# Optimization experiments

Measured on AMD Instinct MI355X. Metric: run time of the kernel, lower is better.

The kernel has to match this reference:

```python
import jax, jax.numpy as jnp
import numpy as np

N = 50000      # nodes
E = 800000     # edges (avg degree 16)
IN_DIM, HID, OUT = 128, 128, 64
EPS = 1e-5     # BatchNorm1d eps


def setup_inputs() -> dict:
    key = jax.random.key(0)
    ks = jax.random.split(key, 8)
    x = jax.random.normal(ks[0], (N, IN_DIM), jnp.float32)
    edge_index = jax.random.randint(ks[1], (2, E), 0, N, dtype=jnp.int32)
    def lin(k, i, o):
        return jax.random.normal(k, (i, o), jnp.float32) / np.sqrt(i).astype(np.float32)
    return {
        "x": x,
        "edge_index": edge_index,
        "W1": lin(ks[2], IN_DIM, HID), "b1": jnp.zeros((HID,), jnp.float32),
        "g1": jnp.ones((HID,), jnp.float32), "beta1": jnp.zeros((HID,), jnp.float32),
        "W2": lin(ks[3], HID, HID), "b2": jnp.zeros((HID,), jnp.float32),
        "g2": jnp.ones((HID,), jnp.float32), "beta2": jnp.zeros((HID,), jnp.float32),
        "W3": lin(ks[4], HID, OUT), "b3": jnp.zeros((OUT,), jnp.float32),
    }


def reference(x, edge_index, W1, b1, g1, beta1, W2, b2, g2, beta2, W3, b3):
    # GCNConv normalization: add self-loops, sym norm D^-1/2 (A+I) D^-1/2
    loops = jnp.arange(N, dtype=edge_index.dtype)
    src = jnp.concatenate([edge_index[0], loops])  # message sources
    dst = jnp.concatenate([edge_index[1], loops])  # aggregation targets
    deg = jax.ops.segment_sum(jnp.ones_like(dst, jnp.float32), dst, num_segments=N)
    dis = jnp.where(deg > 0, jax.lax.rsqrt(jnp.maximum(deg, 1.0)), 0.0)
    norm = dis[src] * dis[dst]  # [E+N]

    def conv(h, W, b):
        h = h @ W  # lin before propagation (PyG GCNConv)
        agg = jax.ops.segment_sum(h[src] * norm[:, None], dst, num_segments=N)
        return agg + b  # bias after aggregation

    def bn(h, g, beta):
        # training-mode BatchNorm1d: batch stats over node dim (biased var)
        m = h.mean(axis=0)
        v = h.var(axis=0)
        return g * (h - m) * jax.lax.rsqrt(v + EPS) + beta

    h = jax.nn.relu(bn(conv(x, W1, b1), g1, beta1))   # dropout deterministic (identity)
    h = jax.nn.relu(bn(conv(h, W2, b2), g2, beta2))
    h = conv(h, W3, b3)
    return jax.nn.log_softmax(h, axis=-1)
```

## Files before the change

kernel.cpp:

```cpp
#include <hip/hip_runtime.h>
#include <hip/hip_fp16.h>
#include <math.h>

#define N_NODES 50000
#define N_EDGES 800000
#define BN_EPS 1e-5f
#define CAP 64

typedef _Float16 f16x8 __attribute__((ext_vector_type(8)));
typedef float f32x4 __attribute__((ext_vector_type(4)));

constexpr int GB = (N_NODES + 63) / 64;
constexpr int FB = 1536;
constexpr int AB = (N_NODES + 3) / 4;

__global__ void setup_k(const float* __restrict__ W1, const float* __restrict__ W2,
                        const float* __restrict__ W3, __half* __restrict__ Wt1,
                        __half* __restrict__ Wt2, __half* __restrict__ Wt3,
                        int* __restrict__ fil, float* __restrict__ sums) {
    int i = blockIdx.x * blockDim.x + threadIdx.x;
    if (i < N_NODES) fil[i] = 0;
    if (i < 512) sums[i] = 0.f;
    if (i < 16384) {
        int k = i >> 7, m = i & 127;
        Wt1[m * 128 + k] = __float2half(W1[i]);
        Wt2[m * 128 + k] = __float2half(W2[i]);
    }
    if (i < 8192) {
        int k = i >> 6, m = i & 63;
        Wt3[m * 128 + k] = __float2half(W3[i]);
    }
}

template <int M, int AF32, int FUSE>
__device__ __forceinline__ void gemm_body(int bid, int tid, __half* Ws,
                                          const void* __restrict__ Av,
                                          const __half* __restrict__ Wt,
                                          const float* __restrict__ scale,
                                          const float* __restrict__ shift,
                                          __half* __restrict__ out) {
    constexpr int NF = M / 32;
    int wid = tid >> 6, lane = tid & 63;

    for (int idx = tid; idx < M * 16; idx += 256) {
        int m = idx >> 4, c = idx & 15;
        *(float4*)(&Ws[m * 136 + c * 8]) = *(const float4*)(&Wt[m * 128 + c * 8]);
    }
    __syncthreads();

    int rbase = bid * 64 + (wid >> 1) * 32;
    int ncol0 = (wid & 1) * (M / 2);
    int koff = (lane >> 4) * 8;

    int arow[2];
#pragma unroll
    for (int mi = 0; mi < 2; ++mi) {
        int r = rbase + mi * 16 + (lane & 15);
        arow[mi] = (r < N_NODES) ? r : (N_NODES - 1);
    }

    f32x4 acc[2][NF];
#pragma unroll
    for (int mi = 0; mi < 2; ++mi)
#pragma unroll
        for (int ni = 0; ni < NF; ++ni) acc[mi][ni] = (f32x4)(0.f);

#pragma unroll
    for (int k0 = 0; k0 < 128; k0 += 32) {
        float scv[8], shv[8];
        if constexpr (FUSE) {
            *(float4*)scv = *(const float4*)(scale + k0 + koff);
            *(float4*)(scv + 4) = *(const float4*)(scale + k0 + koff + 4);
            *(float4*)shv = *(const float4*)(shift + k0 + koff);
            *(float4*)(shv + 4) = *(const float4*)(shift + k0 + koff + 4);
        }
        f16x8 a[2], b[NF];
#pragma unroll
        for (int mi = 0; mi < 2; ++mi) {
            if constexpr (AF32) {
                const float* Af = (const float*)Av + (size_t)arow[mi] * 128 + k0 + koff;
                float4 p0 = *(const float4*)Af;
                float4 p1 = *(const float4*)(Af + 4);
                a[mi][0] = (_Float16)p0.x; a[mi][1] = (_Float16)p0.y;
                a[mi][2] = (_Float16)p0.z; a[mi][3] = (_Float16)p0.w;
                a[mi][4] = (_Float16)p1.x; a[mi][5] = (_Float16)p1.y;
                a[mi][6] = (_Float16)p1.z; a[mi][7] = (_Float16)p1.w;
            } else {
                f16x8 raw = *(const f16x8*)((const __half*)Av + (size_t)arow[mi] * 128 + k0 + koff);
                if constexpr (FUSE) {
#pragma unroll
                    for (int j = 0; j < 8; ++j)
                        a[mi][j] = (_Float16)fmaxf((float)raw[j] * scv[j] + shv[j], 0.f);
                } else {
                    a[mi] = raw;
                }
            }
        }
#pragma unroll
        for (int ni = 0; ni < NF; ++ni)
            b[ni] = *(const f16x8*)(&Ws[(ncol0 + ni * 16 + (lane & 15)) * 136 + k0 + koff]);
#pragma unroll
        for (int mi = 0; mi < 2; ++mi)
#pragma unroll
            for (int ni = 0; ni < NF; ++ni)
                acc[mi][ni] = __builtin_amdgcn_mfma_f32_16x16x32_f16(a[mi], b[ni], acc[mi][ni], 0, 0, 0);
    }

    int ccol = ncol0 + (lane & 15);
#pragma unroll
    for (int mi = 0; mi < 2; ++mi)
#pragma unroll
        for (int q = 0; q < 4; ++q) {
            int grow = rbase + mi * 16 + (lane >> 4) * 4 + q;
            if (grow < N_NODES) {
#pragma unroll
                for (int ni = 0; ni < NF; ++ni)
                    out[(size_t)grow * M + ccol + ni * 16] = __float2half(acc[mi][ni][q]);
            }
        }
}

template <int M, int AF32, int FUSE>
__global__ __launch_bounds__(256) void mfma_gemm_k(const void* __restrict__ Av,
                                                   const __half* __restrict__ Wt,
                                                   const float* __restrict__ scale,
                                                   const float* __restrict__ shift,
                                                   __half* __restrict__ out) {
    __shared__ __half Ws[M * 136];
    gemm_body<M, AF32, FUSE>(blockIdx.x, threadIdx.x, Ws, Av, Wt, scale, shift, out);
}

__global__ __launch_bounds__(256) void gemm1_fill_k(const float* __restrict__ x,
                                                    const __half* __restrict__ Wt1,
                                                    __half* __restrict__ outh,
                                                    const int* __restrict__ ei,
                                                    int* __restrict__ fil,
                                                    int* __restrict__ bkt) {
    __shared__ __half Ws[128 * 136];
    if (blockIdx.x < GB) {
        gemm_body<128, 1, 0>(blockIdx.x, threadIdx.x, Ws, x, Wt1, nullptr, nullptr, outh);
    } else {
        int t = (blockIdx.x - GB) * 256 + threadIdx.x;
        for (int e = t; e < N_EDGES; e += FB * 256) {
            int src = ei[e], dst = ei[N_EDGES + e];
            int pos = atomicAdd(&fil[dst], 1);
            if (pos < CAP) bkt[dst * CAP + pos] = src;
        }
    }
}

__global__ __launch_bounds__(256) void aggh_k(const __half* __restrict__ hs,
                                              const int* __restrict__ fil,
                                              const int* __restrict__ bkt,
                                              const float* __restrict__ bias,
                                              __half* __restrict__ out) {
    int dst = blockIdx.x * 4 + (threadIdx.x >> 6);
    if (dst >= N_NODES) return;
    int lane = threadIdx.x & 63;
    int cnt = fil[dst];
    int n = min(cnt, CAP);
    float dd = rsqrtf((float)cnt + 1.f);
    const __half2* h2 = (const __half2*)hs;
    float2 v = __half22float2(h2[(size_t)dst * 64 + lane]);
    float ax = dd * v.x, ay = dd * v.y;
    const int* bp = bkt + (size_t)dst * CAP;
    int e = 0;
    for (; e + 4 <= n; e += 4) {
        int s0 = bp[e], s1 = bp[e + 1], s2 = bp[e + 2], s3 = bp[e + 3];
        float w0 = rsqrtf((float)fil[s0] + 1.f);
        float w1 = rsqrtf((float)fil[s1] + 1.f);
        float w2 = rsqrtf((float)fil[s2] + 1.f);
        float w3 = rsqrtf((float)fil[s3] + 1.f);
        float2 v0 = __half22float2(h2[(size_t)s0 * 64 + lane]);
        float2 v1 = __half22float2(h2[(size_t)s1 * 64 + lane]);
        float2 v2 = __half22float2(h2[(size_t)s2 * 64 + lane]);
        float2 v3 = __half22float2(h2[(size_t)s3 * 64 + lane]);
        ax += w0 * v0.x + w1 * v1.x + w2 * v2.x + w3 * v3.x;
        ay += w0 * v0.y + w1 * v1.y + w2 * v2.y + w3 * v3.y;
    }
    for (; e < n; ++e) {
        int s = bp[e];
        float w = rsqrtf((float)fil[s] + 1.f);
        float2 vv = __half22float2(h2[(size_t)s * 64 + lane]);
        ax += w * vv.x;
        ay += w * vv.y;
    }
    float2 b = *(const float2*)(bias + lane * 2);
    ((__half2*)out)[(size_t)dst * 64 + lane] =
        __float22half2_rn(make_float2(dd * ax + b.x, dd * ay + b.y));
}

__global__ __launch_bounds__(256) void stats_k(const __half* __restrict__ h,
                                               float* __restrict__ sum, float* __restrict__ sq) {
    __shared__ float ssum[128], ssq[128];
    int tid = threadIdx.x;
    if (tid < 128) { ssum[tid] = 0.f; ssq[tid] = 0.f; }
    __syncthreads();
    float s[8], q[8];
#pragma unroll
    for (int j = 0; j < 8; ++j) { s[j] = 0.f; q[j] = 0.f; }
    const int total = N_NODES * 16;
    int stride = gridDim.x * blockDim.x;
    for (int i = blockIdx.x * blockDim.x + tid; i < total; i += stride) {
        f16x8 v = ((const f16x8*)h)[i];
#pragma unroll
        for (int j = 0; j < 8; ++j) {
            float f = (float)v[j];
            s[j] += f;
            q[j] += f * f;
        }
    }
#pragma unroll
    for (int j = 0; j < 8; ++j) {
        s[j] += __shfl_xor(s[j], 16); s[j] += __shfl_xor(s[j], 32);
        q[j] += __shfl_xor(q[j], 16); q[j] += __shfl_xor(q[j], 32);
    }
    int lane = tid & 63;
    if (lane < 16) {
        int c0 = lane * 8;
#pragma unroll
        for (int j = 0; j < 8; ++j) {
            atomicAdd(&ssum[c0 + j], s[j]);
            atomicAdd(&ssq[c0 + j], q[j]);
        }
    }
    __syncthreads();
    if (tid < 128) {
        atomicAdd(&sum[tid], ssum[tid]);
        atomicAdd(&sq[tid], ssq[tid]);
    }
}

__global__ void finalize_k(const float* __restrict__ sum, const float* __restrict__ sq,
                           const float* __restrict__ g, const float* __restrict__ beta,
                           float* scale, float* shift) {
    int f = threadIdx.x;
    float m = sum[f] * (1.0f / N_NODES);
    float v = sq[f] * (1.0f / N_NODES) - m * m;
    float sc = g[f] * rsqrtf(v + BN_EPS);
    scale[f] = sc;
    shift[f] = beta[f] - m * sc;
}

__global__ __launch_bounds__(256) void agg64sm_k(const __half* __restrict__ hs,
                                                 const int* __restrict__ fil,
                                                 const int* __restrict__ bkt,
                                                 const float* __restrict__ bias,
                                                 float* __restrict__ out) {
    int dst = blockIdx.x * 4 + (threadIdx.x >> 6);
    if (dst >= N_NODES) return;
    int lane = threadIdx.x & 63;
    int cnt = fil[dst];
    int n = min(cnt, CAP);
    float dd = rsqrtf((float)cnt + 1.f);
    float acc = dd * __half2float(hs[(size_t)dst * 64 + lane]);
    const int* bp = bkt + (size_t)dst * CAP;
    int e = 0;
    for (; e + 4 <= n; e += 4) {
        int s0 = bp[e], s1 = bp[e + 1], s2 = bp[e + 2], s3 = bp[e + 3];
        float w0 = rsqrtf((float)fil[s0] + 1.f);
        float w1 = rsqrtf((float)fil[s1] + 1.f);
        float w2 = rsqrtf((float)fil[s2] + 1.f);
        float w3 = rsqrtf((float)fil[s3] + 1.f);
        float v0 = __half2float(hs[(size_t)s0 * 64 + lane]);
        float v1 = __half2float(hs[(size_t)s1 * 64 + lane]);
        float v2 = __half2float(hs[(size_t)s2 * 64 + lane]);
        float v3 = __half2float(hs[(size_t)s3 * 64 + lane]);
        acc += w0 * v0 + w1 * v1 + w2 * v2 + w3 * v3;
    }
    for (; e < n; ++e) {
        int s = bp[e];
        acc += rsqrtf((float)fil[s] + 1.f) * __half2float(hs[(size_t)s * 64 + lane]);
    }
    float v = dd * acc + bias[lane];
    float m = v;
#pragma unroll
    for (int off = 32; off; off >>= 1) m = fmaxf(m, __shfl_xor(m, off));
    float p = expf(v - m);
    float ssum = p;
#pragma unroll
    for (int off = 32; off; off >>= 1) ssum += __shfl_xor(ssum, off);
    out[(size_t)dst * 64 + lane] = v - m - logf(ssum);
}

extern "C" void kernel_launch(void* const* d_in, const int* in_sizes, int n_in,
                              void* d_out, int out_size, void* d_ws, size_t ws_size,
                              hipStream_t stream) {
    const float* x = (const float*)d_in[0];
    const int* ei = (const int*)d_in[1];
    const float* W1 = (const float*)d_in[2];
    const float* b1 = (const float*)d_in[3];
    const float* g1 = (const float*)d_in[4];
    const float* be1 = (const float*)d_in[5];
    const float* W2 = (const float*)d_in[6];
    const float* b2 = (const float*)d_in[7];
    const float* g2 = (const float*)d_in[8];
    const float* be2 = (const float*)d_in[9];
    const float* W3 = (const float*)d_in[10];
    const float* b3 = (const float*)d_in[11];
    float* out = (float*)d_out;

    char* p = (char*)d_ws;
    auto alloc = [&](size_t bytes) {
        void* r = (void*)p;
        p += (bytes + 255) & ~(size_t)255;
        return r;
    };
    int* fil = (int*)alloc(N_NODES * 4);
    int* bkt = (int*)alloc((size_t)N_NODES * CAP * 4);
    float* sums = (float*)alloc(512 * 4);
    float* ss = (float*)alloc(512 * 4);
    __half* Wt1 = (__half*)alloc(128 * 128 * 2);
    __half* Wt2 = (__half*)alloc(128 * 128 * 2);
    __half* Wt3 = (__half*)alloc(64 * 128 * 2);
    __half* bufP = (__half*)alloc((size_t)N_NODES * 128 * 2);
    __half* bufQ = (__half*)alloc((size_t)N_NODES * 128 * 2);

    setup_k<<<196, 256, 0, stream>>>(W1, W2, W3, Wt1, Wt2, Wt3, fil, sums);

    gemm1_fill_k<<<GB + FB, 256, 0, stream>>>(x, Wt1, bufQ, ei, fil, bkt);
    aggh_k<<<AB, 256, 0, stream>>>(bufQ, fil, bkt, b1, bufP);
    stats_k<<<1024, 256, 0, stream>>>(bufP, sums, sums + 128);
    finalize_k<<<1, 128, 0, stream>>>(sums, sums + 128, g1, be1, ss, ss + 128);

    mfma_gemm_k<128, 0, 1><<<GB, 256, 0, stream>>>(bufP, Wt2, ss, ss + 128, bufQ);
    aggh_k<<<AB, 256, 0, stream>>>(bufQ, fil, bkt, b2, bufP);
    stats_k<<<1024, 256, 0, stream>>>(bufP, sums + 256, sums + 384);
    finalize_k<<<1, 128, 0, stream>>>(sums + 256, sums + 384, g2, be2, ss + 256, ss + 384);

    mfma_gemm_k<64, 0, 1><<<GB, 256, 0, stream>>>(bufP, Wt3, ss + 256, ss + 384, bufQ);
    agg64sm_k<<<AB, 256, 0, stream>>>(bufQ, fil, bkt, b3, out);
}
```

Before: 281.5 us.

## Precompute degree norms, fold source scaling into GEMM epilogue, shrink bucket indices

Adds a kernel that precomputes D^-1/2 per node once. Layers 2 and 3 scale the GEMM output rows by the source normalisation, so the aggregation kernels no longer need per-edge weight gathers and reduce to plain sums. Bucket indices are stored as 16-bit values, which halves index traffic; this only holds because N fits in 16 bits. The GEMM now reads weights directly from global memory instead of staging them in LDS, and the fill/GEMM1 block order is swapped. Reading weights from global memory may cost extra load latency.

New measurement: 276.5 us. Within noise of the previous version (-1.8%).

```diff
diff --git a/kernel.cpp b/kernel.cpp
--- a/kernel.cpp
+++ b/kernel.cpp
@@ -32,21 +32,16 @@
     }
 }
 
-template <int M, int AF32, int FUSE>
-__device__ __forceinline__ void gemm_body(int bid, int tid, __half* Ws,
+template <int M, int AF32, int FUSE, int DSCALE>
+__device__ __forceinline__ void gemm_body(int bid, int tid,
                                           const void* __restrict__ Av,
                                           const __half* __restrict__ Wt,
                                           const float* __restrict__ scale,
                                           const float* __restrict__ shift,
+                                          const float* __restrict__ dis,
                                           __half* __restrict__ out) {
     constexpr int NF = M / 32;
     int wid = tid >> 6, lane = tid & 63;
-
-    for (int idx = tid; idx < M * 16; idx += 256) {
-        int m = idx >> 4, c = idx & 15;
-        *(float4*)(&Ws[m * 136 + c * 8]) = *(const float4*)(&Wt[m * 128 + c * 8]);
-    }
-    __syncthreads();
 
     int rbase = bid * 64 + (wid >> 1) * 32;
     int ncol0 = (wid & 1) * (M / 2);
@@ -98,7 +93,7 @@
         }
 #pragma unroll
         for (int ni = 0; ni < NF; ++ni)
-            b[ni] = *(const f16x8*)(&Ws[(ncol0 + ni * 16 + (lane & 15)) * 136 + k0 + koff]);
+            b[ni] = *(const f16x8*)(Wt + (size_t)(ncol0 + ni * 16 + (lane & 15)) * 128 + k0 + koff);
 #pragma unroll
         for (int mi = 0; mi < 2; ++mi)
 #pragma unroll
@@ -113,75 +108,86 @@
         for (int q = 0; q < 4; ++q) {
             int grow = rbase + mi * 16 + (lane >> 4) * 4 + q;
             if (grow < N_NODES) {
+                float ds = DSCALE ? dis[grow] : 1.0f;
 #pragma unroll
                 for (int ni = 0; ni < NF; ++ni)
-                    out[(size_t)grow * M + ccol + ni * 16] = __float2half(acc[mi][ni][q]);
+                    out[(size_t)grow * M + ccol + ni * 16] = __float2half(acc[mi][ni][q] * ds);
             }
         }
 }
 
-template <int M, int AF32, int FUSE>
+template <int M, int AF32, int FUSE, int DSCALE>
 __global__ __launch_bounds__(256) void mfma_gemm_k(const void* __restrict__ Av,
                                                    const __half* __restrict__ Wt,
                                                    const float* __restrict__ scale,
                                                    const float* __restrict__ shift,
+                                                   const float* __restrict__ dis,
                                                    __half* __restrict__ out) {
-    __shared__ __half Ws[M * 136];
-    gemm_body<M, AF32, FUSE>(blockIdx.x, threadIdx.x, Ws, Av, Wt, scale, shift, out);
-}
-
-__global__ __launch_bounds__(256) void gemm1_fill_k(const float* __restrict__ x,
+    gemm_body<M, AF32, FUSE, DSCALE>(blockIdx.x, threadIdx.x, Av, Wt, scale, shift, dis, out);
+}
+
+__global__ __launch_bounds__(256) void fill_gemm1_k(const float* __restrict__ x,
                                                     const __half* __restrict__ Wt1,
                                                     __half* __restrict__ outh,
                                                     const int* __restrict__ ei,
                                                     int* __restrict__ fil,
-                                                    int* __restrict__ bkt) {
-    __shared__ __half Ws[128 * 136];
-    if (blockIdx.x < GB) {
-        gemm_body<128, 1, 0>(blockIdx.x, threadIdx.x, Ws, x, Wt1, nullptr, nullptr, outh);
-    } else {
-        int t = (blockIdx.x - GB) * 256 + threadIdx.x;
+                                                    unsigned short* __restrict__ bkt) {
+    if (blockIdx.x < FB) {
+        int t = blockIdx.x * 256 + threadIdx.x;
         for (int e = t; e < N_EDGES; e += FB * 256) {
             int src = ei[e], dst = ei[N_EDGES + e];
             int pos = atomicAdd(&fil[dst], 1);
-            if (pos < CAP) bkt[dst * CAP + pos] = src;
-        }
-    }
-}
-
+            if (pos < CAP) bkt[dst * CAP + pos] = (unsigned short)src;
+        }
+    } else {
+        gemm_body<128, 1, 0, 0>(blockIdx.x - FB, threadIdx.x, x, Wt1, nullptr, nullptr,
+                                nullptr, outh);
+    }
+}
+
+__global__ void dis_k(const int* __restrict__ fil, float* __restrict__ dis) {
+    int i = blockIdx.x * blockDim.x + threadIdx.x;
+    if (i < N_NODES) dis[i] = rsqrtf((float)fil[i] + 1.f);
+}
+
+template <int SRCDIS>
 __global__ __launch_bounds__(256) void aggh_k(const __half* __restrict__ hs,
                                               const int* __restrict__ fil,
-                                              const int* __restrict__ bkt,
+                                              const unsigned short* __restrict__ bkt,
+                                              const float* __restrict__ dis,
                                               const float* __restrict__ bias,
                                               __half* __restrict__ out) {
     int dst = blockIdx.x * 4 + (threadIdx.x >> 6);
     if (dst >= N_NODES) return;
     int lane = threadIdx.x & 63;
-    int cnt = fil[dst];
-    int n = min(cnt, CAP);
-    float dd = rsqrtf((float)cnt + 1.f);
+    int n = min(fil[dst], CAP);
+    float dd = dis[dst];
     const __half2* h2 = (const __half2*)hs;
     float2 v = __half22float2(h2[(size_t)dst * 64 + lane]);
-    float ax = dd * v.x, ay = dd * v.y;
-    const int* bp = bkt + (size_t)dst * CAP;
+    float ax, ay;
+    if constexpr (SRCDIS) { ax = dd * v.x; ay = dd * v.y; }
+    else { ax = v.x; ay = v.y; }
+    const unsigned short* bp = bkt + (size_t)dst * CAP;
     int e = 0;
     for (; e + 4 <= n; e += 4) {
         int s0 = bp[e], s1 = bp[e + 1], s2 = bp[e + 2], s3 = bp[e + 3];
-        float w0 = rsqrtf((float)fil[s0] + 1.f);
-        float w1 = rsqrtf((float)fil[s1] + 1.f);
-        float w2 = rsqrtf((float)fil[s2] + 1.f);
-        float w3 = rsqrtf((float)fil[s3] + 1.f);
         float2 v0 = __half22float2(h2[(size_t)s0 * 64 + lane]);
         float2 v1 = __half22float2(h2[(size_t)s1 * 64 + lane]);
         float2 v2 = __half22float2(h2[(size_t)s2 * 64 + lane]);
         float2 v3 = __half22float2(h2[(size_t)s3 * 64 + lane]);
-        ax += w0 * v0.x + w1 * v1.x + w2 * v2.x + w3 * v3.x;
-        ay += w0 * v0.y + w1 * v1.y + w2 * v2.y + w3 * v3.y;
+        if constexpr (SRCDIS) {
+            float w0 = dis[s0], w1 = dis[s1], w2 = dis[s2], w3 = dis[s3];
+            ax += w0 * v0.x + w1 * v1.x + w2 * v2.x + w3 * v3.x;
+            ay += w0 * v0.y + w1 * v1.y + w2 * v2.y + w3 * v3.y;
+        } else {
+            ax += (v0.x + v1.x) + (v2.x + v3.x);
+            ay += (v0.y + v1.y) + (v2.y + v3.y);
+        }
     }
     for (; e < n; ++e) {
         int s = bp[e];
-        float w = rsqrtf((float)fil[s] + 1.f);
         float2 vv = __half22float2(h2[(size_t)s * 64 + lane]);
+        float w = SRCDIS ? dis[s] : 1.0f;
         ax += w * vv.x;
         ay += w * vv.y;
     }
@@ -244,34 +250,27 @@
 
 __global__ __launch_bounds__(256) void agg64sm_k(const __half* __restrict__ hs,
                                                  const int* __restrict__ fil,
-                                                 const int* __restrict__ bkt,
+                                                 const unsigned short* __restrict__ bkt,
+                                                 const float* __restrict__ dis,
                                                  const float* __restrict__ bias,
                                                  float* __restrict__ out) {
     int dst = blockIdx.x * 4 + (threadIdx.x >> 6);
     if (dst >= N_NODES) return;
     int lane = threadIdx.x & 63;
-    int cnt = fil[dst];
-    int n = min(cnt, CAP);
-    float dd = rsqrtf((float)cnt + 1.f);
-    float acc = dd * __half2float(hs[(size_t)dst * 64 + lane]);
-    const int* bp = bkt + (size_t)dst * CAP;
+    int n = min(fil[dst], CAP);
+    float dd = dis[dst];
+    float acc = __half2float(hs[(size_t)dst * 64 + lane]);
+    const unsigned short* bp = bkt + (size_t)dst * CAP;
     int e = 0;
     for (; e + 4 <= n; e += 4) {
         int s0 = bp[e], s1 = bp[e + 1], s2 = bp[e + 2], s3 = bp[e + 3];
-        float w0 = rsqrtf((float)fil[s0] + 1.f);
-        float w1 = rsqrtf((float)fil[s1] + 1.f);
-        float w2 = rsqrtf((float)fil[s2] + 1.f);
-        float w3 = rsqrtf((float)fil[s3] + 1.f);
         float v0 = __half2float(hs[(size_t)s0 * 64 + lane]);
         float v1 = __half2float(hs[(size_t)s1 * 64 + lane]);
         float v2 = __half2float(hs[(size_t)s2 * 64 + lane]);
         float v3 = __half2float(hs[(size_t)s3 * 64 + lane]);
-        acc += w0 * v0 + w1 * v1 + w2 * v2 + w3 * v3;
-    }
-    for (; e < n; ++e) {
-        int s = bp[e];
-        acc += rsqrtf((float)fil[s] + 1.f) * __half2float(hs[(size_t)s * 64 + lane]);
-    }
+        acc += (v0 + v1) + (v2 + v3);
+    }
+    for (; e < n; ++e) acc += __half2float(hs[(size_t)bp[e] * 64 + lane]);
     float v = dd * acc + bias[lane];
     float m = v;
 #pragma unroll
@@ -307,7 +306,8 @@
         return r;
     };
     int* fil = (int*)alloc(N_NODES * 4);
-    int* bkt = (int*)alloc((size_t)N_NODES * CAP * 4);
+    unsigned short* bkt = (unsigned short*)alloc((size_t)N_NODES * CAP * 2);
+    float* dis = (float*)alloc(N_NODES * 4);
     float* sums = (float*)alloc(512 * 4);
     float* ss = (float*)alloc(512 * 4);
     __half* Wt1 = (__half*)alloc(128 * 128 * 2);
@@ -318,16 +318,17 @@
 
     setup_k<<<196, 256, 0, stream>>>(W1, W2, W3, Wt1, Wt2, Wt3, fil, sums);
 
-    gemm1_fill_k<<<GB + FB, 256, 0, stream>>>(x, Wt1, bufQ, ei, fil, bkt);
-    aggh_k<<<AB, 256, 0, stream>>>(bufQ, fil, bkt, b1, bufP);
+    fill_gemm1_k<<<FB + GB, 256, 0, stream>>>(x, Wt1, bufQ, ei, fil, bkt);
+    dis_k<<<196, 256, 0, stream>>>(fil, dis);
+    aggh_k<1><<<AB, 256, 0, stream>>>(bufQ, fil, bkt, dis, b1, bufP);
     stats_k<<<1024, 256, 0, stream>>>(bufP, sums, sums + 128);
     finalize_k<<<1, 128, 0, stream>>>(sums, sums + 128, g1, be1, ss, ss + 128);
 
-    mfma_gemm_k<128, 0, 1><<<GB, 256, 0, stream>>>(bufP, Wt2, ss, ss + 128, bufQ);
-    aggh_k<<<AB, 256, 0, stream>>>(bufQ, fil, bkt, b2, bufP);
+    mfma_gemm_k<128, 0, 1, 1><<<GB, 256, 0, stream>>>(bufP, Wt2, ss, ss + 128, dis, bufQ);
+    aggh_k<0><<<AB, 256, 0, stream>>>(bufQ, fil, bkt, dis, b2, bufP);
     stats_k<<<1024, 256, 0, stream>>>(bufP, sums + 256, sums + 384);
     finalize_k<<<1, 128, 0, stream>>>(sums + 256, sums + 384, g2, be2, ss + 256, ss + 384);
 
-    mfma_gemm_k<64, 0, 1><<<GB, 256, 0, stream>>>(bufP, Wt3, ss + 256, ss + 384, bufQ);
-    agg64sm_k<<<AB, 256, 0, stream>>>(bufQ, fil, bkt, b3, out);
-}
+    mfma_gemm_k<64, 0, 1, 1><<<GB, 256, 0, stream>>>(bufP, Wt3, ss + 256, ss + 384, dis, bufQ);
+    agg64sm_k<<<AB, 256, 0, stream>>>(bufQ, fil, bkt, dis, b3, out);
+}
```
